# Kernel tuning notes

Hardware: AMD Instinct MI355X
Metric: run time of the kernel (lower is better)

Reference implementation:

```python
import jax, jax.numpy as jnp
import numpy as np

N_A = 100000; N_B = 100000; E = 1600000
H = 128; OUT = 16; G = 256; D_A = 64; D_B = 32


def setup_inputs() -> dict:
    key = jax.random.key(0)
    ks = jax.random.split(key, 24)
    f32 = jnp.float32
    def w(k, shape, fan_in):
        return jax.random.normal(k, shape, dtype=f32) / np.sqrt(fan_in)
    inp = {
        'x_a': jax.random.normal(ks[0], (N_A, D_A), dtype=f32),
        'x_b': jax.random.normal(ks[1], (N_B, D_B), dtype=f32),
        'ei_ab': jax.random.randint(ks[2], (2, E), 0, N_A),  # row0: src in a, row1: dst in b
        'ei_ba': jax.random.randint(ks[3], (2, E), 0, N_B),
        'ei_aa': jax.random.randint(ks[4], (2, E), 0, N_A),
        'batch_a': jnp.sort(jax.random.randint(ks[5], (N_A,), 0, G)),
        'batch_b': jnp.sort(jax.random.randint(ks[6], (N_B,), 0, G)),
        # node-type input embeddings
        'Wemb_a': w(ks[7], (D_A, H), D_A), 'bemb_a': jnp.zeros((H,), f32),
        'Wemb_b': w(ks[8], (D_B, H), D_B), 'bemb_b': jnp.zeros((H,), f32),
        # SAGEConv params per relation: lin_l (with bias) on aggregated, lin_r (no bias) on root
        'Wl_ab': w(ks[9], (H, H), H), 'bl_ab': jnp.zeros((H,), f32), 'Wr_ab': w(ks[10], (H, H), H),
        'Wl_ba': w(ks[11], (H, H), H), 'bl_ba': jnp.zeros((H,), f32), 'Wr_ba': w(ks[12], (H, H), H),
        'Wl_aa': w(ks[13], (H, H), H), 'bl_aa': jnp.zeros((H,), f32), 'Wr_aa': w(ks[14], (H, H), H),
        # output head
        'Wout': w(ks[15], (H, OUT), H), 'bout': jnp.zeros((OUT,), f32),
    }
    return inp


def _sage(x_src, x_dst, ei, Wl, bl, Wr, n_dst):
    # mean aggregation of source features over incoming edges, then transform + root
    msg = x_src[ei[0]]                                        # [E, H] gather
    s = jax.ops.segment_sum(msg, ei[1], num_segments=n_dst)   # [n_dst, H]
    cnt = jax.ops.segment_sum(jnp.ones((ei.shape[1], 1), x_src.dtype), ei[1], num_segments=n_dst)
    agg = s / jnp.maximum(cnt, 1.0)
    return agg @ Wl + bl + x_dst @ Wr


def _mean_pool(x, batch, num_graphs):
    s = jax.ops.segment_sum(x, batch, num_segments=num_graphs)
    cnt = jax.ops.segment_sum(jnp.ones((x.shape[0], 1), x.dtype), batch, num_segments=num_graphs)
    return s / jnp.maximum(cnt, 1.0)


def reference(x_a, x_b, ei_ab, ei_ba, ei_aa, batch_a, batch_b,
              Wemb_a, bemb_a, Wemb_b, bemb_b,
              Wl_ab, bl_ab, Wr_ab, Wl_ba, bl_ba, Wr_ba, Wl_aa, bl_aa, Wr_aa,
              Wout, bout):
    # per-type input projection
    h_a = x_a @ Wemb_a + bemb_a            # [N_A, H]
    h_b = x_b @ Wemb_b + bemb_b            # [N_B, H]
    # HeteroConv: one SAGEConv per relation, mean over relations per dst type
    m_b = _sage(h_a, h_b, ei_ab, Wl_ab, bl_ab, Wr_ab, N_B)          # dst 'b': 1 relation
    m_a1 = _sage(h_b, h_a, ei_ba, Wl_ba, bl_ba, Wr_ba, N_A)
    m_a2 = _sage(h_a, h_a, ei_aa, Wl_aa, bl_aa, Wr_aa, N_A)
    h_a2 = 0.5 * (m_a1 + m_a2)                                      # dst 'a': mean of 2 relations
    h_b2 = m_b
    # ReLU + per-type global mean pool + mean over node types
    p_a = _mean_pool(jax.nn.relu(h_a2), batch_a, G)                 # [G, H]
    p_b = _mean_pool(jax.nn.relu(h_b2), batch_b, G)
    x = 0.5 * (p_a + p_b)
    return x @ Wout + bout                                          # [G, OUT]
```

## Files before the change

### kernel.cpp

```cpp
#include <hip/hip_runtime.h>

#define NA 100000
#define NB 100000
#define NEDGE 1600000
#define HD 128
#define OUTD 16
#define NG 256
#define DA 64
#define DB 32

#define BIN_SHIFT 9
#define BIN_W 512
#define NBINS_R 196
#define NBINS 588
#define PADBIN 10240
#define EPB 8192
#define ECHUNKS 196

typedef unsigned int uint_t;
typedef unsigned short ushort_t;
typedef unsigned char uchar_t;
typedef __bf16 bf16_t;
typedef bf16_t bf16x8 __attribute__((ext_vector_type(8)));
typedef float f32x4 __attribute__((ext_vector_type(4)));
typedef float f32x2 __attribute__((ext_vector_type(2)));

__device__ __forceinline__ float bflo(uint_t u) {
    union { uint_t i; float f; } c; c.i = u << 16; return c.f;
}
__device__ __forceinline__ float bfhi(uint_t u) {
    union { uint_t i; float f; } c; c.i = u & 0xffff0000u; return c.f;
}
__device__ __forceinline__ float bf2f(ushort_t u) {
    union { uint_t i; float f; } c; c.i = ((uint_t)u) << 16; return c.f;
}
__device__ __forceinline__ uint_t f2bf(float f) {
    union { float f; uint_t i; } c; c.f = f;
    uint_t r = c.i + 0x7FFFu + ((c.i >> 16) & 1u);
    return r >> 16;
}
__device__ __forceinline__ uint_t pack2bf(float lo, float hi) {
    return f2bf(lo) | (f2bf(hi) << 16);
}
__device__ __forceinline__ uchar_t f2fp8(float v) {
    return (uchar_t)(__builtin_amdgcn_cvt_pk_fp8_f32(v, v, 0, false) & 0xff);
}

__global__ void __launch_bounds__(256)
prep_misc_kernel(const float* __restrict__ Wl_ab, const float* __restrict__ Wr_ab,
                 const float* __restrict__ Wl_ba, const float* __restrict__ Wl_aa,
                 const float* __restrict__ Wr_ba, const float* __restrict__ Wr_aa,
                 const float* __restrict__ Wemb_a, const float* __restrict__ Wemb_b,
                 ushort_t* __restrict__ wt_fb, ushort_t* __restrict__ wt_pa,
                 ushort_t* __restrict__ wt_ea, ushort_t* __restrict__ wt_eb,
                 const float* __restrict__ bl_ba, const float* __restrict__ bl_aa,
                 float* __restrict__ bias_pa,
                 const int* __restrict__ batch_a, const int* __restrict__ batch_b,
                 float* __restrict__ ga, float* __restrict__ gb)
{
    const int bx = blockIdx.x;
    __align__(16) ushort_t tmp[8];
    if (bx >= 40) {
        if (bx <= 43) {
            const int id = (bx - 40) * 256 + threadIdx.x;
            const int kk = id >> 9, ni = (id >> 6) & 7, l = id & 63;
            const int col = ni * 16 + (l & 15);
            const int k0 = kk * 32 + (l >> 4) * 8;
#pragma unroll
            for (int j = 0; j < 8; ++j) tmp[j] = (ushort_t)f2bf(Wemb_a[(k0 + j) * HD + col]);
            *reinterpret_cast<uint4*>(wt_ea + (size_t)id * 8) = *reinterpret_cast<const uint4*>(tmp);
            return;
        }
        if (bx <= 45) {
            const int id = (bx - 44) * 256 + threadIdx.x;
            const int ni = id >> 6, l = id & 63;
            const int col = ni * 16 + (l & 15);
            const int k0 = (l >> 4) * 8;
#pragma unroll
            for (int j = 0; j < 8; ++j) tmp[j] = (ushort_t)f2bf(Wemb_b[(k0 + j) * HD + col]);
            *reinterpret_cast<uint4*>(wt_eb + (size_t)id * 8) = *reinterpret_cast<const uint4*>(tmp);
            return;
        }
        if (bx == 46) {
            if (threadIdx.x < HD) bias_pa[threadIdx.x] = bl_ba[threadIdx.x] + bl_aa[threadIdx.x];
            return;
        }
        const int g = threadIdx.x;
        const int* batch = (bx == 48) ? batch_b : batch_a;
        float* outp = (bx == 48) ? gb : ga;
        const int n = NA;
        int lo0 = 0, hi0 = n;
        while (lo0 < hi0) { const int mid = (lo0 + hi0) >> 1; if (batch[mid] < g) lo0 = mid + 1; else hi0 = mid; }
        int lo1 = 0, hi1 = n;
        while (lo1 < hi1) { const int mid = (lo1 + hi1) >> 1; if (batch[mid] < g + 1) lo1 = mid + 1; else hi1 = mid; }
        outp[g] = (float)(lo1 - lo0);
        return;
    }
    const int m = bx >> 3;
    const int id = (bx & 7) * 256 + threadIdx.x;
    const int kk = id >> 9, ni = (id >> 6) & 7, l = id & 63;
    const int col = ni * 16 + (l & 15);
    const int k0 = kk * 32 + (l >> 4) * 8;
    const float* src = (m == 0) ? Wl_ab : (m == 1) ? Wr_ab : (m == 2) ? Wl_ba
                     : (m == 3) ? Wl_aa : Wr_ba;
#pragma unroll
    for (int j = 0; j < 8; ++j) {
        float v = src[(k0 + j) * HD + col];
        if (m == 4) v += Wr_aa[(k0 + j) * HD + col];
        tmp[j] = (ushort_t)f2bf(v);
    }
    const int half = ni >> 2, nih = ni & 3;
    const size_t eoff = (size_t)half * 8192 + ((kk * 4 + nih) * 64 + l) * 8;
    ushort_t* dst = (m < 2) ? (wt_fb + (size_t)m * 16384) : (wt_pa + (size_t)(m - 2) * 16384);
    *reinterpret_cast<uint4*>(dst + eoff) = *reinterpret_cast<const uint4*>(tmp);
}

template<int K>
__device__ __forceinline__ void
emb_body(const float* __restrict__ x, const ushort_t* __restrict__ wtf,
         const float* __restrict__ bias, ushort_t* __restrict__ h,
         uchar_t* __restrict__ h8, int n, ushort_t* wlds)
{
    constexpr int KST = K / 32;
    for (int i = threadIdx.x * 8; i < K * HD; i += 2048)
        *reinterpret_cast<uint4*>(wlds + i) = *reinterpret_cast<const uint4*>(wtf + i);
    __syncthreads();

    const int l = threadIdx.x & 63, w = threadIdx.x >> 6;
    const int lo = l & 15, hi = l >> 4;
    const int row_base = blockIdx.x * 128 + w * 32;

    f32x4 acc[2][8];
    const f32x4 zero = {0.f, 0.f, 0.f, 0.f};
#pragma unroll
    for (int mi = 0; mi < 2; ++mi)
#pragma unroll
        for (int ni = 0; ni < 8; ++ni) acc[mi][ni] = zero;

    bf16x8 a[2][KST];
#pragma unroll
    for (int mi = 0; mi < 2; ++mi) {
        int r = row_base + mi * 16 + lo;
        r = min(r, n - 1);
        const float* xr = x + (size_t)r * K + hi * 8;
#pragma unroll
        for (int kk = 0; kk < KST; ++kk) {
            const float4 f0 = *reinterpret_cast<const float4*>(xr + kk * 32);
            const float4 f1 = *reinterpret_cast<const float4*>(xr + kk * 32 + 4);
            __align__(16) ushort_t us[8];
            us[0] = (ushort_t)f2bf(f0.x); us[1] = (ushort_t)f2bf(f0.y);
            us[2] = (ushort_t)f2bf(f0.z); us[3] = (ushort_t)f2bf(f0.w);
            us[4] = (ushort_t)f2bf(f1.x); us[5] = (ushort_t)f2bf(f1.y);
            us[6] = (ushort_t)f2bf(f1.z); us[7] = (ushort_t)f2bf(f1.w);
            a[mi][kk] = *reinterpret_cast<const bf16x8*>(us);
        }
    }
#pragma unroll
    for (int kk = 0; kk < KST; ++kk) {
#pragma unroll
        for (int ni = 0; ni < 8; ++ni) {
            const bf16x8 b = *reinterpret_cast<const bf16x8*>(wlds + ((kk * 8 + ni) * 64 + l) * 8);
            acc[0][ni] = __builtin_amdgcn_mfma_f32_16x16x32_bf16(a[0][kk], b, acc[0][ni], 0, 0, 0);
            acc[1][ni] = __builtin_amdgcn_mfma_f32_16x16x32_bf16(a[1][kk], b, acc[1][ni], 0, 0, 0);
        }
    }
#pragma unroll
    for (int ni = 0; ni < 8; ++ni) {
        const int col = ni * 16 + lo;
        const float bv = bias[col];
#pragma unroll
        for (int mi = 0; mi < 2; ++mi) {
            const f32x4 v = acc[mi][ni];
#pragma unroll
            for (int r = 0; r < 4; ++r) {
                const int row = row_base + mi * 16 + hi * 4 + r;
                if (row < n) {
                    const float val = v[r] + bv;
                    h[(size_t)row * HD + col] = (ushort_t)f2bf(val);
                    h8[(size_t)row * HD + col] = f2fp8(val);
                }
            }
        }
    }
}

__global__ void __launch_bounds__(256)
emb2_kernel(const float* __restrict__ x_a, const float* __restrict__ x_b,
            const ushort_t* __restrict__ wt_ea, const ushort_t* __restrict__ wt_eb,
            const float* __restrict__ bemb_a, const float* __restrict__ bemb_b,
            ushort_t* __restrict__ h_a, ushort_t* __restrict__ h_b,
            uchar_t* __restrict__ h8_a, uchar_t* __restrict__ h8_b)
{
    __shared__ ushort_t wlds[DA * HD];
    if (blockIdx.y == 0) emb_body<DA>(x_a, wt_ea, bemb_a, h_a, h8_a, NA, wlds);
    else                 emb_body<DB>(x_b, wt_eb, bemb_b, h_b, h8_b, NB, wlds);
}

__global__ void __launch_bounds__(256)
part3_kernel(const int* __restrict__ ei_ab, const int* __restrict__ ei_ba,
             const int* __restrict__ ei_aa, int* __restrict__ bincnt,
             uint_t* __restrict__ binned)
{
    __shared__ uint_t sorted[EPB];
    __shared__ int lh[NBINS_R];
    __shared__ int lbase[NBINS_R];
    __shared__ int gbase[NBINS_R];
    __shared__ int lcur[NBINS_R];
    __shared__ int sc[256];
    const int r = blockIdx.y;
    const int* ei = (r == 0) ? ei_ab : (r == 1) ? ei_ba : ei_aa;
    const int t = threadIdx.x;
    for (int i = t; i < NBINS_R; i += 256) lh[i] = 0;
    __syncthreads();
    const int e0 = blockIdx.x * EPB;
    const int e1 = min(e0 + EPB, NEDGE);
    for (int e = e0 + t; e < e1; e += 256)
        atomicAdd(&lh[ei[NEDGE + e] >> BIN_SHIFT], 1);
    __syncthreads();
    {
        const int v = (t < NBINS_R) ? lh[t] : 0;
        sc[t] = v; __syncthreads();
        for (int d = 1; d < 256; d <<= 1) {
            const int x = (t >= d) ? sc[t - d] : 0;
            __syncthreads();
            sc[t] += x;
            __syncthreads();
        }
        if (t < NBINS_R) {
            const int ex = sc[t] - v;
            lbase[t] = ex; lcur[t] = ex;
            gbase[t] = v ? atomicAdd(&bincnt[r * NBINS_R + t], v) : 0;
        }
    }
    __syncthreads();
    for (int e = e0 + t; e < e1; e += 256) {
        const int dst = ei[NEDGE + e];
        const int src = ei[e];
        const int bin = dst >> BIN_SHIFT;
        const int pos = atomicAdd(&lcur[bin], 1);
        sorted[pos] = ((uint_t)(dst & (BIN_W - 1)) << 17) | (uint_t)src;
    }
    __syncthreads();
    const int wid = t >> 6, lane = t & 63;
    for (int b = wid; b < NBINS_R; b += 4) {
        const int cnt = lh[b], lb = lbase[b];
        uint_t* dst = binned + (size_t)(r * NBINS_R + b) * PADBIN + gbase[b];
        for (int k = lane; k < cnt; k += 64) dst[k] = sorted[lb + k];
    }
}

__global__ void __launch_bounds__(256)
binfill3_kernel(const uint_t* __restrict__ binned, const int* __restrict__ bincnt,
                int* __restrict__ off3, int* __restrict__ cnt3, int* __restrict__ csr3)
{
    __shared__ int hist[BIN_W];
    __shared__ int A[BIN_W];
    __shared__ int cursor[BIN_W];
    const int b = blockIdx.x;
    const int r = blockIdx.y;
    const int g = r * NBINS_R + b;
    const int start = g * PADBIN;
    const int end = start + bincnt[g];
    const int t = threadIdx.x;
    const int i0 = t, i1 = t + 256;
    hist[i0] = 0; hist[i1] = 0;
    __syncthreads();
    for (int j = start + t; j < end; j += 256)
        atomicAdd(&hist[binned[j] >> 17], 1);
    __syncthreads();
    A[i0] = hist[i0]; A[i1] = hist[i1];
    __syncthreads();
    for (int d = 1; d < BIN_W; d <<= 1) {
        const int x0 = (i0 >= d) ? A[i0 - d] : 0;
        const int x1 = (i1 >= d) ? A[i1 - d] : 0;
        __syncthreads();
        A[i0] += x0; A[i1] += x1;
        __syncthreads();
    }
    const int node0 = b * BIN_W;
#pragma unroll
    for (int q = 0; q < 2; ++q) {
        const int i = t + q * 256;
        const int ex = start + A[i] - hist[i];
        cursor[i] = ex;
        const int node = node0 + i;
        if (node < NA) { off3[r * NA + node] = ex; cnt3[r * NA + node] = hist[i]; }
    }
    __syncthreads();
    for (int j = start + t; j < end; j += 256) {
        const uint_t p = binned[j];
        const int pos = atomicAdd(&cursor[p >> 17], 1);
        csr3[pos] = (int)(p & 0x1FFFFu);
    }
}

__global__ void __launch_bounds__(256)
gather3_kernel(const uchar_t* __restrict__ h8_a, const uchar_t* __restrict__ h8_b,
               const int* __restrict__ csr3, const int* __restrict__ off3,
               const int* __restrict__ cnt3,
               ushort_t* __restrict__ s_ab, ushort_t* __restrict__ s_ba,
               ushort_t* __restrict__ s_aa)
{
    const int r = blockIdx.y;
    const uchar_t* hsrc = (r == 1) ? h8_b : h8_a;
    ushort_t* s = (r == 0) ? s_ab : (r == 1) ? s_ba : s_aa;
    const int* off = off3 + r * NA;
    const int* cnt = cnt3 + r * NA;
    const int wid = threadIdx.x >> 6, lane = threadIdx.x & 63;
    const int hl = lane & 31;
    const int sel = (lane >> 5) & 1;
    const int nw = gridDim.x * 4;
    for (int node = blockIdx.x * 4 + wid; node < NA; node += nw) {
        const int o0 = off[node], deg = cnt[node];
        const int o1 = o0 + deg;
        f32x2 acc01 = {0.f, 0.f}, acc23 = {0.f, 0.f};
        int j = o0;
        for (; j + 16 <= o1; j += 16) {
            uint_t vv[8];
#pragma unroll
            for (int q = 0; q < 8; ++q) {
                const int sE = csr3[j + 2 * q + sel];
                vv[q] = *reinterpret_cast<const uint_t*>(hsrc + (size_t)sE * HD + hl * 4);
            }
#pragma unroll
            for (int q = 0; q < 8; ++q) {
                acc01 += __builtin_amdgcn_cvt_pk_f32_fp8(vv[q], false);
                acc23 += __builtin_amdgcn_cvt_pk_f32_fp8(vv[q], true);
            }
        }
        for (; j + 4 <= o1; j += 4) {
            uint_t vv[2];
#pragma unroll
            for (int q = 0; q < 2; ++q) {
                const int sE = csr3[j + 2 * q + sel];
                vv[q] = *reinterpret_cast<const uint_t*>(hsrc + (size_t)sE * HD + hl * 4);
            }
#pragma unroll
            for (int q = 0; q < 2; ++q) {
                acc01 += __builtin_amdgcn_cvt_pk_f32_fp8(vv[q], false);
                acc23 += __builtin_amdgcn_cvt_pk_f32_fp8(vv[q], true);
            }
        }
        for (; j + 2 <= o1; j += 2) {
            const int sE = csr3[j + sel];
            const uint_t v = *reinterpret_cast<const uint_t*>(hsrc + (size_t)sE * HD + hl * 4);
            acc01 += __builtin_amdgcn_cvt_pk_f32_fp8(v, false);
            acc23 += __builtin_amdgcn_cvt_pk_f32_fp8(v, true);
        }
        if (j < o1) {
            const int sE = csr3[min(j + sel, o1 - 1)];
            const uint_t v = *reinterpret_cast<const uint_t*>(hsrc + (size_t)sE * HD + hl * 4);
            if (!sel) {
                acc01 += __builtin_amdgcn_cvt_pk_f32_fp8(v, false);
                acc23 += __builtin_amdgcn_cvt_pk_f32_fp8(v, true);
            }
        }
        float ax0 = acc01[0], ax1 = acc01[1], ax2 = acc23[0], ax3 = acc23[1];
        ax0 += __shfl_xor(ax0, 32); ax1 += __shfl_xor(ax1, 32);
        ax2 += __shfl_xor(ax2, 32); ax3 += __shfl_xor(ax3, 32);
        if (!sel) {
            const float inv = 1.0f / fmaxf((float)deg, 1.0f);
            uint2 wv;
            wv.x = pack2bf(ax0 * inv, ax1 * inv);
            wv.y = pack2bf(ax2 * inv, ax3 * inv);
            *reinterpret_cast<uint2*>(s + (size_t)node * HD + hl * 4) = wv;
        }
    }
}

template<int NSRC, int SCALE_HALF>
__device__ __forceinline__ void
mfma_body(const ushort_t* __restrict__ x0, const ushort_t* __restrict__ x1,
          const ushort_t* __restrict__ x2,
          const ushort_t* __restrict__ wtf, const float* __restrict__ bias,
          ushort_t* __restrict__ m_out, int n, int tile, int half, char* smem)
{
    ushort_t* wlds = (ushort_t*)smem;
    for (int i = threadIdx.x * 8; i < NSRC * 8192; i += 2048) {
        const int s = i >> 13, off = i & 8191;
        *reinterpret_cast<uint4*>(wlds + i) =
            *reinterpret_cast<const uint4*>(wtf + (size_t)s * 16384 + half * 8192 + off);
    }
    __syncthreads();

    const int l  = threadIdx.x & 63, w = threadIdx.x >> 6;
    const int lo = l & 15, hi = l >> 4;
    const int row_base = tile * 128 + w * 32;

    f32x4 acc[2][4];
    const f32x4 zero = {0.f, 0.f, 0.f, 0.f};
#pragma unroll
    for (int mi = 0; mi < 2; ++mi)
#pragma unroll
        for (int ni = 0; ni < 4; ++ni) acc[mi][ni] = zero;

#pragma unroll
    for (int s = 0; s < NSRC; ++s) {
        const ushort_t* xs = (s == 0) ? x0 : (s == 1) ? x1 : x2;
        bf16x8 a[2][4];
#pragma unroll
        for (int mi = 0; mi < 2; ++mi) {
            int r = row_base + mi * 16 + lo;
            r = min(r, n - 1);
            const ushort_t* xr = xs + (size_t)r * HD + hi * 8;
#pragma unroll
            for (int kk = 0; kk < 4; ++kk)
                a[mi][kk] = *reinterpret_cast<const bf16x8*>(xr + kk * 32);
        }
        const ushort_t* wm = wlds + s * 8192;
#pragma unroll
        for (int kk = 0; kk < 4; ++kk) {
#pragma unroll
            for (int nih = 0; nih < 4; ++nih) {
                const bf16x8 b = *reinterpret_cast<const bf16x8*>(wm + ((kk * 4 + nih) * 64 + l) * 8);
                acc[0][nih] = __builtin_amdgcn_mfma_f32_16x16x32_bf16(a[0][kk], b, acc[0][nih], 0, 0, 0);
                acc[1][nih] = __builtin_amdgcn_mfma_f32_16x16x32_bf16(a[1][kk], b, acc[1][nih], 0, 0, 0);
            }
        }
    }

#pragma unroll
    for (int nih = 0; nih < 4; ++nih) {
        const int col = half * 64 + nih * 16 + lo;
        const float bv = bias[col];
#pragma unroll
        for (int mi = 0; mi < 2; ++mi) {
            const f32x4 v = acc[mi][nih];
#pragma unroll
            for (int r = 0; r < 4; ++r) {
                const int row = row_base + mi * 16 + hi * 4 + r;
                if (row < n) {
                    float val = v[r] + bv;
                    if (SCALE_HALF) val *= 0.5f;
                    m_out[(size_t)row * HD + col] = (ushort_t)f2bf(fmaxf(val, 0.f));
                }
            }
        }
    }
}

__global__ void __launch_bounds__(256)
mfma_merged(const ushort_t* __restrict__ s_ab, const ushort_t* __restrict__ h_b,
            const ushort_t* __restrict__ wt_fb, const float* __restrict__ bl_ab,
            ushort_t* __restrict__ m_b,
            const ushort_t* __restrict__ s_ba, const ushort_t* __restrict__ s_aa,
            const ushort_t* __restrict__ h_a,
            const ushort_t* __restrict__ wt_pa, const float* __restrict__ bias_pa,
            ushort_t* __restrict__ m_a)
{
    extern __shared__ char smem[];
    const int u = blockIdx.x;
    const int tile = (u >> 4) * 8 + (u & 7);
    const int half = (u >> 3) & 1;
    if (tile >= (NA + 127) / 128) return;
    if (blockIdx.y == 0)
        mfma_body<2, 0>(s_ab, h_b, nullptr, wt_fb, bl_ab, m_b, NB, tile, half, smem);
    else
        mfma_body<3, 1>(s_ba, s_aa, h_a, wt_pa, bias_pa, m_a, NA, tile, half, smem);
}

__global__ void __launch_bounds__(256)
pool_kernel(const ushort_t* __restrict__ m_a, const ushort_t* __restrict__ m_b,
            const int* __restrict__ batch_a, const int* __restrict__ batch_b,
            float* __restrict__ pool_a, float* __restrict__ pool_b)
{
    const ushort_t* m = blockIdx.y ? m_b : m_a;
    const int* batch = blockIdx.y ? batch_b : batch_a;
    float* pool = blockIdx.y ? pool_b : pool_a;
    const int col = threadIdx.x & 127;
    const int rh = threadIdx.x >> 7;
    int row = blockIdx.x * 128 + rh * 64;
    const int rend = min(row + 64, NA);
    if (row >= rend) return;
    float acc = 0.f;
    int gcur = batch[row];
    for (; row < rend; ++row) {
        const int g = batch[row];
        if (g != gcur) {
            unsafeAtomicAdd(pool + (size_t)gcur * HD + col, acc);
            acc = 0.f; gcur = g;
        }
        acc += bf2f(m[(size_t)row * HD + col]);
    }
    unsafeAtomicAdd(pool + (size_t)gcur * HD + col, acc);
}

__global__ void final_kernel(const float* __restrict__ pa, const float* __restrict__ pb,
                             const float* __restrict__ ga, const float* __restrict__ gb,
                             const float* __restrict__ Wout, const float* __restrict__ bout,
                             float* __restrict__ out)
{
    const int g = blockIdx.x;
    const int lane = threadIdx.x;
    const float inva = 1.0f / fmaxf(ga[g], 1.0f);
    const float invb = 1.0f / fmaxf(gb[g], 1.0f);
    if (lane < OUTD) {
        float acc = bout[lane];
        for (int k = 0; k < HD; ++k) {
            const float x = 0.5f * (pa[g * HD + k] * inva + pb[g * HD + k] * invb);
            acc = fmaf(x, Wout[k * OUTD + lane], acc);
        }
        out[g * OUTD + lane] = acc;
    }
}

extern "C" void kernel_launch(void* const* d_in, const int* in_sizes, int n_in,
                              void* d_out, int out_size, void* d_ws, size_t ws_size,
                              hipStream_t stream)
{
    const float* x_a     = (const float*)d_in[0];
    const float* x_b     = (const float*)d_in[1];
    const int*   ei_ab   = (const int*)d_in[2];
    const int*   ei_ba   = (const int*)d_in[3];
    const int*   ei_aa   = (const int*)d_in[4];
    const int*   batch_a = (const int*)d_in[5];
    const int*   batch_b = (const int*)d_in[6];
    const float* Wemb_a  = (const float*)d_in[7];
    const float* bemb_a  = (const float*)d_in[8];
    const float* Wemb_b  = (const float*)d_in[9];
    const float* bemb_b  = (const float*)d_in[10];
    const float* Wl_ab   = (const float*)d_in[11];
    const float* bl_ab   = (const float*)d_in[12];
    const float* Wr_ab   = (const float*)d_in[13];
    const float* Wl_ba   = (const float*)d_in[14];
    const float* bl_ba   = (const float*)d_in[15];
    const float* Wr_ba   = (const float*)d_in[16];
    const float* Wl_aa   = (const float*)d_in[17];
    const float* bl_aa   = (const float*)d_in[18];
    const float* Wr_aa   = (const float*)d_in[19];
    const float* Wout    = (const float*)d_in[20];
    const float* bout    = (const float*)d_in[21];
    float* out = (float*)d_out;

    char* p = (char*)d_ws;
    ushort_t* h_a  = (ushort_t*)p; p += (size_t)NA * HD * 2;
    ushort_t* h_b  = (ushort_t*)p; p += (size_t)NB * HD * 2;
    ushort_t* s_ab = (ushort_t*)p; p += (size_t)NB * HD * 2;
    ushort_t* s_ba = (ushort_t*)p; p += (size_t)NA * HD * 2;
    ushort_t* s_aa = (ushort_t*)p; p += (size_t)NA * HD * 2;
    ushort_t* m_a  = (ushort_t*)p; p += (size_t)NA * HD * 2;
    ushort_t* m_b  = (ushort_t*)p; p += (size_t)NB * HD * 2;
    uchar_t* h8_a  = (uchar_t*)p;  p += (size_t)NA * HD;
    uchar_t* h8_b  = (uchar_t*)p;  p += (size_t)NB * HD;
    int* csr3   = (int*)p;  p += (size_t)NBINS * PADBIN * 4;
    uint_t* binned = (uint_t*)p; p += (size_t)NBINS * PADBIN * 4;
    int* off3   = (int*)p;  p += (size_t)3 * NA * 4;
    int* cnt3   = (int*)p;  p += (size_t)3 * NA * 4;
    int* bincnt = (int*)p;  p += (NBINS + 4) * 4;
    float* pool_a = (float*)p; p += (size_t)NG * HD * 4;
    float* pool_b = (float*)p; p += (size_t)NG * HD * 4;
    float* gcnt_a = (float*)p; p += NG * 4;
    float* gcnt_b = (float*)p; p += NG * 4;
    ushort_t* wt_fb = (ushort_t*)p; p += 2 * 16384 * 2;
    ushort_t* wt_pa = (ushort_t*)p; p += 3 * 16384 * 2;
    ushort_t* wt_ea = (ushort_t*)p; p += 64 * HD * 2;
    ushort_t* wt_eb = (ushort_t*)p; p += 32 * HD * 2;
    float* bias_pa  = (float*)p;    p += HD * 4;

    const int GT = (NA + 127) / 128;

    hipMemsetAsync(pool_a, 0, (size_t)2 * NG * HD * 4, stream);
    hipMemsetAsync(bincnt, 0, (size_t)NBINS * 4, stream);

    prep_misc_kernel<<<49, 256, 0, stream>>>(Wl_ab, Wr_ab, Wl_ba, Wl_aa, Wr_ba, Wr_aa,
                                             Wemb_a, Wemb_b, wt_fb, wt_pa, wt_ea, wt_eb,
                                             bl_ba, bl_aa, bias_pa,
                                             batch_a, batch_b, gcnt_a, gcnt_b);

    emb2_kernel<<<dim3(GT, 2), 256, 0, stream>>>(x_a, x_b, wt_ea, wt_eb, bemb_a, bemb_b,
                                                 h_a, h_b, h8_a, h8_b);

    part3_kernel<<<dim3(ECHUNKS, 3), 256, 0, stream>>>(ei_ab, ei_ba, ei_aa, bincnt, binned);
    binfill3_kernel<<<dim3(NBINS_R, 3), 256, 0, stream>>>(binned, bincnt, off3, cnt3, csr3);

    gather3_kernel<<<dim3(2048, 3), 256, 0, stream>>>(h8_a, h8_b, csr3, off3, cnt3, s_ab, s_ba, s_aa);

    const int lds_m = 3 * 16384;
    hipFuncSetAttribute((const void*)mfma_merged, hipFuncAttributeMaxDynamicSharedMemorySize, lds_m);
    const int GX = ((2 * GT + 15) / 16) * 16;
    mfma_merged<<<dim3(GX, 2), 256, lds_m, stream>>>(s_ab, h_b, wt_fb, bl_ab, m_b,
                                                     s_ba, s_aa, h_a, wt_pa, bias_pa, m_a);

    pool_kernel<<<dim3((NA + 127) / 128, 2), 256, 0, stream>>>(m_a, m_b, batch_a, batch_b, pool_a, pool_b);

    final_kernel<<<NG, 64, 0, stream>>>(pool_a, pool_b, gcnt_a, gcnt_b, Wout, bout, out);
}
```

Before: 399.7 us.

## Fuse per-bin CSR build into gather kernel using LDS-resident edge lists

Removes the separate binfill kernel and its global csr3/off3/cnt3 arrays. Each gather block now owns one 512-node bin: it builds the histogram, prefix sum and scattered edge list in shared memory (about 46KB), then gathers the fp8 source rows for those nodes. The gather lane mapping also changes from 32 lanes×4 bytes to 16 lanes×8 bytes, with 4 edges in flight per wave. The cost is only 588 blocks of 512 threads with large LDS use, which limits occupancy and latency hiding for the random gathers. Uneven bin sizes may also leave blocks imbalanced.

New measurement: 383.5 us. 1.04x faster.

```diff
diff --git a/kernel.cpp b/kernel.cpp
--- a/kernel.cpp
+++ b/kernel.cpp
@@ -249,121 +249,113 @@
     }
 }
 
-__global__ void __launch_bounds__(256)
-binfill3_kernel(const uint_t* __restrict__ binned, const int* __restrict__ bincnt,
-                int* __restrict__ off3, int* __restrict__ cnt3, int* __restrict__ csr3)
-{
-    __shared__ int hist[BIN_W];
-    __shared__ int A[BIN_W];
-    __shared__ int cursor[BIN_W];
-    const int b = blockIdx.x;
-    const int r = blockIdx.y;
-    const int g = r * NBINS_R + b;
-    const int start = g * PADBIN;
-    const int end = start + bincnt[g];
-    const int t = threadIdx.x;
-    const int i0 = t, i1 = t + 256;
-    hist[i0] = 0; hist[i1] = 0;
-    __syncthreads();
-    for (int j = start + t; j < end; j += 256)
-        atomicAdd(&hist[binned[j] >> 17], 1);
-    __syncthreads();
-    A[i0] = hist[i0]; A[i1] = hist[i1];
-    __syncthreads();
-    for (int d = 1; d < BIN_W; d <<= 1) {
-        const int x0 = (i0 >= d) ? A[i0 - d] : 0;
-        const int x1 = (i1 >= d) ? A[i1 - d] : 0;
-        __syncthreads();
-        A[i0] += x0; A[i1] += x1;
-        __syncthreads();
-    }
-    const int node0 = b * BIN_W;
-#pragma unroll
-    for (int q = 0; q < 2; ++q) {
-        const int i = t + q * 256;
-        const int ex = start + A[i] - hist[i];
-        cursor[i] = ex;
-        const int node = node0 + i;
-        if (node < NA) { off3[r * NA + node] = ex; cnt3[r * NA + node] = hist[i]; }
-    }
-    __syncthreads();
-    for (int j = start + t; j < end; j += 256) {
-        const uint_t p = binned[j];
-        const int pos = atomicAdd(&cursor[p >> 17], 1);
-        csr3[pos] = (int)(p & 0x1FFFFu);
-    }
-}
-
-__global__ void __launch_bounds__(256)
+__global__ void __launch_bounds__(512)
 gather3_kernel(const uchar_t* __restrict__ h8_a, const uchar_t* __restrict__ h8_b,
-               const int* __restrict__ csr3, const int* __restrict__ off3,
-               const int* __restrict__ cnt3,
+               const uint_t* __restrict__ binned, const int* __restrict__ bincnt,
                ushort_t* __restrict__ s_ab, ushort_t* __restrict__ s_ba,
                ushort_t* __restrict__ s_aa)
 {
-    const int r = blockIdx.y;
+    __shared__ int hist[BIN_W];
+    __shared__ int off[BIN_W];
+    __shared__ int cursor[BIN_W];
+    __shared__ uint_t eLDS[PADBIN];
+    const int b = blockIdx.x, r = blockIdx.y;
+    const int g = r * NBINS_R + b;
     const uchar_t* hsrc = (r == 1) ? h8_b : h8_a;
     ushort_t* s = (r == 0) ? s_ab : (r == 1) ? s_ba : s_aa;
-    const int* off = off3 + r * NA;
-    const int* cnt = cnt3 + r * NA;
-    const int wid = threadIdx.x >> 6, lane = threadIdx.x & 63;
-    const int hl = lane & 31;
-    const int sel = (lane >> 5) & 1;
-    const int nw = gridDim.x * 4;
-    for (int node = blockIdx.x * 4 + wid; node < NA; node += nw) {
-        const int o0 = off[node], deg = cnt[node];
+    const int t = threadIdx.x;
+    const int ecnt = bincnt[g];
+    const uint_t* bsrc = binned + (size_t)g * PADBIN;
+
+    hist[t] = 0;
+    __syncthreads();
+    for (int j = t; j < ecnt; j += 512)
+        atomicAdd(&hist[bsrc[j] >> 17], 1);
+    __syncthreads();
+    const int v = hist[t];
+    off[t] = v;
+    __syncthreads();
+    for (int d = 1; d < 512; d <<= 1) {
+        const int x = (t >= d) ? off[t - d] : 0;
+        __syncthreads();
+        off[t] += x;
+        __syncthreads();
+    }
+    const int ex = off[t] - v;
+    __syncthreads();
+    off[t] = ex;
+    cursor[t] = ex;
+    __syncthreads();
+    for (int j = t; j < ecnt; j += 512) {
+        const uint_t p = bsrc[j];
+        const int pos = atomicAdd(&cursor[p >> 17], 1);
+        eLDS[pos] = p & 0x1FFFFu;
+    }
+    __syncthreads();
+
+    const int wid = t >> 6, lane = t & 63;
+    const int hl = lane & 15;
+    const int sel = lane >> 4;
+    const int node0 = b * BIN_W;
+    for (int nl = wid; nl < BIN_W; nl += 8) {
+        const int node = node0 + nl;
+        if (node >= NA) break;
+        const int o0 = off[nl], deg = hist[nl];
         const int o1 = o0 + deg;
-        f32x2 acc01 = {0.f, 0.f}, acc23 = {0.f, 0.f};
+        f32x2 a01 = {0.f, 0.f}, a23 = {0.f, 0.f}, a45 = {0.f, 0.f}, a67 = {0.f, 0.f};
         int j = o0;
-        for (; j + 16 <= o1; j += 16) {
-            uint_t vv[8];
-#pragma unroll
-            for (int q = 0; q < 8; ++q) {
-                const int sE = csr3[j + 2 * q + sel];
-                vv[q] = *reinterpret_cast<const uint_t*>(hsrc + (size_t)sE * HD + hl * 4);
+        for (; j + 8 <= o1; j += 8) {
+            uint2 vv[2];
+#pragma unroll
+            for (int q = 0; q < 2; ++q) {
+                const int sE = (int)eLDS[j + 4 * q + sel];
+                vv[q] = *reinterpret_cast<const uint2*>(hsrc + (size_t)sE * HD + hl * 8);
             }
 #pragma unroll
-            for (int q = 0; q < 8; ++q) {
-                acc01 += __builtin_amdgcn_cvt_pk_f32_fp8(vv[q], false);
-                acc23 += __builtin_amdgcn_cvt_pk_f32_fp8(vv[q], true);
+            for (int q = 0; q < 2; ++q) {
+                a01 += __builtin_amdgcn_cvt_pk_f32_fp8(vv[q].x, false);
+                a23 += __builtin_amdgcn_cvt_pk_f32_fp8(vv[q].x, true);
+                a45 += __builtin_amdgcn_cvt_pk_f32_fp8(vv[q].y, false);
+                a67 += __builtin_amdgcn_cvt_pk_f32_fp8(vv[q].y, true);
             }
         }
         for (; j + 4 <= o1; j += 4) {
-            uint_t vv[2];
-#pragma unroll
-            for (int q = 0; q < 2; ++q) {
-                const int sE = csr3[j + 2 * q + sel];
-                vv[q] = *reinterpret_cast<const uint_t*>(hsrc + (size_t)sE * HD + hl * 4);
+            const int sE = (int)eLDS[j + sel];
+            const uint2 vv = *reinterpret_cast<const uint2*>(hsrc + (size_t)sE * HD + hl * 8);
+            a01 += __builtin_amdgcn_cvt_pk_f32_fp8(vv.x, false);
+            a23 += __builtin_amdgcn_cvt_pk_f32_fp8(vv.x, true);
+            a45 += __builtin_amdgcn_cvt_pk_f32_fp8(vv.y, false);
+            a67 += __builtin_amdgcn_cvt_pk_f32_fp8(vv.y, true);
+        }
+        if (j < o1) {
+            const int rem = o1 - j;
+            const int sE = (int)eLDS[min(j + sel, o1 - 1)];
+            const uint2 vv = *reinterpret_cast<const uint2*>(hsrc + (size_t)sE * HD + hl * 8);
+            if (sel < rem) {
+                a01 += __builtin_amdgcn_cvt_pk_f32_fp8(vv.x, false);
+                a23 += __builtin_amdgcn_cvt_pk_f32_fp8(vv.x, true);
+                a45 += __builtin_amdgcn_cvt_pk_f32_fp8(vv.y, false);
+                a67 += __builtin_amdgcn_cvt_pk_f32_fp8(vv.y, true);
             }
-#pragma unroll
-            for (int q = 0; q < 2; ++q) {
-                acc01 += __builtin_amdgcn_cvt_pk_f32_fp8(vv[q], false);
-                acc23 += __builtin_amdgcn_cvt_pk_f32_fp8(vv[q], true);
-            }
-        }
-        for (; j + 2 <= o1; j += 2) {
-            const int sE = csr3[j + sel];
-            const uint_t v = *reinterpret_cast<const uint_t*>(hsrc + (size_t)sE * HD + hl * 4);
-            acc01 += __builtin_amdgcn_cvt_pk_f32_fp8(v, false);
-            acc23 += __builtin_amdgcn_cvt_pk_f32_fp8(v, true);
-        }
-        if (j < o1) {
-            const int sE = csr3[min(j + sel, o1 - 1)];
-            const uint_t v = *reinterpret_cast<const uint_t*>(hsrc + (size_t)sE * HD + hl * 4);
-            if (!sel) {
-                acc01 += __builtin_amdgcn_cvt_pk_f32_fp8(v, false);
-                acc23 += __builtin_amdgcn_cvt_pk_f32_fp8(v, true);
-            }
-        }
-        float ax0 = acc01[0], ax1 = acc01[1], ax2 = acc23[0], ax3 = acc23[1];
-        ax0 += __shfl_xor(ax0, 32); ax1 += __shfl_xor(ax1, 32);
-        ax2 += __shfl_xor(ax2, 32); ax3 += __shfl_xor(ax3, 32);
-        if (!sel) {
+        }
+        float f0 = a01[0], f1 = a01[1], f2 = a23[0], f3 = a23[1];
+        float f4 = a45[0], f5 = a45[1], f6 = a67[0], f7 = a67[1];
+        f0 += __shfl_xor(f0, 16); f0 += __shfl_xor(f0, 32);
+        f1 += __shfl_xor(f1, 16); f1 += __shfl_xor(f1, 32);
+        f2 += __shfl_xor(f2, 16); f2 += __shfl_xor(f2, 32);
+        f3 += __shfl_xor(f3, 16); f3 += __shfl_xor(f3, 32);
+        f4 += __shfl_xor(f4, 16); f4 += __shfl_xor(f4, 32);
+        f5 += __shfl_xor(f5, 16); f5 += __shfl_xor(f5, 32);
+        f6 += __shfl_xor(f6, 16); f6 += __shfl_xor(f6, 32);
+        f7 += __shfl_xor(f7, 16); f7 += __shfl_xor(f7, 32);
+        if (sel == 0) {
             const float inv = 1.0f / fmaxf((float)deg, 1.0f);
-            uint2 wv;
-            wv.x = pack2bf(ax0 * inv, ax1 * inv);
-            wv.y = pack2bf(ax2 * inv, ax3 * inv);
-            *reinterpret_cast<uint2*>(s + (size_t)node * HD + hl * 4) = wv;
+            uint4 wv;
+            wv.x = pack2bf(f0 * inv, f1 * inv);
+            wv.y = pack2bf(f2 * inv, f3 * inv);
+            wv.z = pack2bf(f4 * inv, f5 * inv);
+            wv.w = pack2bf(f6 * inv, f7 * inv);
+            *reinterpret_cast<uint4*>(s + (size_t)node * HD + hl * 8) = wv;
         }
     }
 }
@@ -542,10 +534,7 @@
     ushort_t* m_b  = (ushort_t*)p; p += (size_t)NB * HD * 2;
     uchar_t* h8_a  = (uchar_t*)p;  p += (size_t)NA * HD;
     uchar_t* h8_b  = (uchar_t*)p;  p += (size_t)NB * HD;
-    int* csr3   = (int*)p;  p += (size_t)NBINS * PADBIN * 4;
     uint_t* binned = (uint_t*)p; p += (size_t)NBINS * PADBIN * 4;
-    int* off3   = (int*)p;  p += (size_t)3 * NA * 4;
-    int* cnt3   = (int*)p;  p += (size_t)3 * NA * 4;
     int* bincnt = (int*)p;  p += (NBINS + 4) * 4;
     float* pool_a = (float*)p; p += (size_t)NG * HD * 4;
     float* pool_b = (float*)p; p += (size_t)NG * HD * 4;
@@ -571,9 +560,8 @@
                                                  h_a, h_b, h8_a, h8_b);
 
     part3_kernel<<<dim3(ECHUNKS, 3), 256, 0, stream>>>(ei_ab, ei_ba, ei_aa, bincnt, binned);
-    binfill3_kernel<<<dim3(NBINS_R, 3), 256, 0, stream>>>(binned, bincnt, off3, cnt3, csr3);
-
-    gather3_kernel<<<dim3(2048, 3), 256, 0, stream>>>(h8_a, h8_b, csr3, off3, cnt3, s_ab, s_ba, s_aa);
+    gather3_kernel<<<dim3(NBINS_R, 3), 512, 0, stream>>>(h8_a, h8_b, binned, bincnt,
+                                                         s_ab, s_ba, s_aa);
 
     const int lds_m = 3 * 16384;
     hipFuncSetAttribute((const void*)mfma_merged, hipFuncAttributeMaxDynamicSharedMemorySize, lds_m);
```
